# Performance work log

Measured on AMD Instinct MI355X. Metric: run time of the kernel, lower is better.

## Reference

```python
import jax, jax.numpy as jnp
import numpy as np

N_HEADS = 8
D_K = 64
SCALE = D_K ** (-0.5)


def setup_inputs() -> dict:
    key = jax.random.key(0)
    k1, k2, k3 = jax.random.split(key, 3)
    B, C, H, W = 8, 512, 32, 32
    x = jax.random.normal(k1, (B, C, H, W), dtype=jnp.float32)
    # Linear weights stored as [in, out] so y = x @ W + b (same math as torch Linear)
    W_qkv = jax.random.normal(k2, (C, N_HEADS * D_K * 3), dtype=jnp.float32) * (1.0 / np.sqrt(C))
    b_qkv = jnp.zeros((N_HEADS * D_K * 3,), dtype=jnp.float32)
    W_out = jax.random.normal(k3, (N_HEADS * D_K, C), dtype=jnp.float32) * (1.0 / np.sqrt(N_HEADS * D_K))
    b_out = jnp.zeros((C,), dtype=jnp.float32)
    return {"x": x, "W_qkv": W_qkv, "b_qkv": b_qkv, "W_out": W_out, "b_out": b_out}


def reference(x, W_qkv, b_qkv, W_out, b_out):
    B, C, H, W = x.shape
    N = H * W
    # [B, C, H, W] -> [B, N, C]  (tokens are spatial positions)
    xf = jnp.transpose(x.reshape(B, C, N), (0, 2, 1))
    # NOTE: the original forward never applies self.norm, so neither do we.
    qkv = xf @ W_qkv + b_qkv                       # [B, N, 3*h*d]
    qkv = qkv.reshape(B, N, N_HEADS, 3 * D_K)
    q, k, v = jnp.split(qkv, 3, axis=-1)           # each [B, N, h, d]
    attn = jnp.einsum('bihd,bjhd->bijh', q, k) * SCALE
    attn = jax.nn.softmax(attn, axis=2)            # softmax over key index j
    res = jnp.einsum('bijh,bjhd->bihd', attn, v)   # [B, N, h, d]
    res = res.reshape(B, N, N_HEADS * D_K)
    res = res @ W_out + b_out
    res = res + xf                                 # residual
    res = jnp.transpose(res, (0, 2, 1)).reshape(B, C, H, W)
    return res
```

## Files before the change

### kernel.cpp

```cpp
#include <hip/hip_runtime.h>
#include <hip/hip_bf16.h>
#include <cstdint>

typedef __bf16 bf16;
typedef __attribute__((ext_vector_type(8))) __bf16 bf16x8;
typedef __attribute__((ext_vector_type(4))) __bf16 bf16x4;
typedef __attribute__((ext_vector_type(4))) float f32x4;

#define CEXP 0.1803368801111244f

__global__ __launch_bounds__(256) void prep_all(const float* __restrict__ x,
                                                const float* __restrict__ Wqkv,
                                                const float* __restrict__ Wout,
                                                bf16* __restrict__ xT,
                                                bf16* __restrict__ WqkvT,
                                                bf16* __restrict__ WoutT) {
  __shared__ bf16 t[32][33];
  const int z = blockIdx.z;
  const float* src;
  bf16* dst;
  int C;
  if (z < 8) {
    if (blockIdx.x >= 32) return;
    src = x + (size_t)z * 512 * 1024;
    dst = xT + (size_t)z * 1024 * 512;
    C = 1024;
  } else if (z == 8) {
    src = Wqkv; dst = WqkvT; C = 1536;
  } else {
    if (blockIdx.x >= 16) return;
    src = Wout; dst = WoutT; C = 512;
  }
  const int c0 = blockIdx.x * 32, r0 = blockIdx.y * 32;
  const int tx = threadIdx.x, ty = threadIdx.y;
#pragma unroll
  for (int i = 0; i < 4; ++i)
    t[ty + i * 8][tx] = (bf16)src[(size_t)(r0 + ty + i * 8) * C + c0 + tx];
  __syncthreads();
#pragma unroll
  for (int i = 0; i < 4; ++i)
    dst[(size_t)(c0 + ty + i * 8) * 512 + r0 + tx] = t[tx][ty + i * 8];
}

__global__ __launch_bounds__(256) void gemm_qkv(const bf16* __restrict__ xT,
                                                const bf16* __restrict__ WqkvT,
                                                const float* __restrict__ bqkv,
                                                bf16* __restrict__ Qb,
                                                bf16* __restrict__ Kb,
                                                bf16* __restrict__ Vb) {
  __shared__ bf16 As[128 * 72];
  __shared__ bf16 Bs[128 * 72];
  const int b = blockIdx.z;
  const int m0 = blockIdx.y * 128;
  const int co0 = blockIdx.x * 128;
  const int tid = threadIdx.x;
  const int w = tid >> 6, l = tid & 63;
  const int wr = w >> 1, wc = w & 1;
  const int quad = l >> 4, l16 = l & 15;

  const bf16* A = xT + (size_t)b * 1024 * 512;

  f32x4 acc[4][4];
#pragma unroll
  for (int i = 0; i < 4; ++i)
#pragma unroll
    for (int j = 0; j < 4; ++j) acc[i][j] = (f32x4){0.f, 0.f, 0.f, 0.f};

  const int srow = w * 32 + (l >> 3);
  const int scol = (l & 7) * 8;

  for (int kk = 0; kk < 8; ++kk) {
    const int k0 = kk * 64;
    bf16x8 av[4], bv[4];
#pragma unroll
    for (int i = 0; i < 4; ++i) {
      av[i] = *(const bf16x8*)&A[(size_t)(m0 + srow + i * 8) * 512 + k0 + scol];
      bv[i] = *(const bf16x8*)&WqkvT[(size_t)(co0 + srow + i * 8) * 512 + k0 + scol];
    }
#pragma unroll
    for (int i = 0; i < 4; ++i) {
      *(bf16x8*)&As[(srow + i * 8) * 72 + scol] = av[i];
      *(bf16x8*)&Bs[(srow + i * 8) * 72 + scol] = bv[i];
    }
    __syncthreads();
#pragma unroll
    for (int ks = 0; ks < 2; ++ks) {
      bf16x8 a[4], bb[4];
#pragma unroll
      for (int rb = 0; rb < 4; ++rb)
        a[rb] = *(const bf16x8*)&As[(wr * 64 + rb * 16 + l16) * 72 + ks * 32 + quad * 8];
#pragma unroll
      for (int cb = 0; cb < 4; ++cb)
        bb[cb] = *(const bf16x8*)&Bs[(wc * 64 + cb * 16 + l16) * 72 + ks * 32 + quad * 8];
#pragma unroll
      for (int rb = 0; rb < 4; ++rb)
#pragma unroll
        for (int cb = 0; cb < 4; ++cb)
          acc[rb][cb] = __builtin_amdgcn_mfma_f32_16x16x32_bf16(a[rb], bb[cb], acc[rb][cb], 0, 0, 0);
    }
    __syncthreads();
  }

#pragma unroll
  for (int cb = 0; cb < 4; ++cb) {
    const int co = co0 + wc * 64 + cb * 16 + l16;
    const int h = co / 192;
    const int rem = co - h * 192;
    const int part = rem >> 6;
    const int dd = rem & 63;
    const float bias = bqkv[co];
    if (part == 2) {
      bf16* base = Vb + ((size_t)(b * 8 + h) * 64 + dd) * 1024;
#pragma unroll
      for (int rb = 0; rb < 4; ++rb) {
        const int n = m0 + wr * 64 + rb * 16 + quad * 4;
        f32x4 v = acc[rb][cb];
        bf16x4 ov;
#pragma unroll
        for (int r = 0; r < 4; ++r) ov[r] = (bf16)(v[r] + bias);
        *(bf16x4*)&base[n] = ov;
      }
    } else {
      const float sc = (part == 0) ? CEXP : 1.0f;
      bf16* dst = (part == 0) ? Qb : Kb;
      bf16* base = dst + ((size_t)(b * 8 + h) * 1024) * 64 + dd;
#pragma unroll
      for (int rb = 0; rb < 4; ++rb) {
        const int n = m0 + wr * 64 + rb * 16 + quad * 4;
        f32x4 v = acc[rb][cb];
#pragma unroll
        for (int r = 0; r < 4; ++r) base[(size_t)(n + r) * 64] = (bf16)((v[r] + bias) * sc);
      }
    }
  }
}

__global__ __launch_bounds__(256) void attn_k(const bf16* __restrict__ Qb,
                                              const bf16* __restrict__ Kb,
                                              const bf16* __restrict__ Vb,
                                              bf16* __restrict__ Ob) {
  __shared__ bf16 Ks[128 * 72];
  __shared__ bf16 Vs[64 * 136];
  const int bh = blockIdx.x;
  const int b = bh >> 3, h = bh & 7;
  const int q0 = blockIdx.y * 128;
  const int tid = threadIdx.x;
  const int w = tid >> 6, l = tid & 63;
  const int quad = l >> 4, l16 = l & 15;

  const bf16* Qg = Qb + (size_t)bh * 1024 * 64;
  const bf16* Kg = Kb + (size_t)bh * 1024 * 64;
  const bf16* Vg = Vb + (size_t)bh * 64 * 1024;

  bf16x8 qb[2][2];
#pragma unroll
  for (int mt = 0; mt < 2; ++mt)
#pragma unroll
    for (int ks = 0; ks < 2; ++ks)
      qb[mt][ks] = *(const bf16x8*)&Qg[(size_t)(q0 + w * 32 + mt * 16 + l16) * 64 + ks * 32 + quad * 8];

  bf16x8 ones;
#pragma unroll
  for (int e = 0; e < 8; ++e) ones[e] = (bf16)1.0f;

  f32x4 o[2][4], acc_l[2];
#pragma unroll
  for (int mt = 0; mt < 2; ++mt) {
    acc_l[mt] = (f32x4){0.f, 0.f, 0.f, 0.f};
#pragma unroll
    for (int db = 0; db < 4; ++db) o[mt][db] = (f32x4){0.f, 0.f, 0.f, 0.f};
  }

  const int kr = tid >> 1, kc = (tid & 1) * 32;
  const int vr = tid >> 2, vc = (tid & 3) * 32;

  bf16x8 ka[4], va[4];
#pragma unroll
  for (int e = 0; e < 4; ++e) {
    ka[e] = *(const bf16x8*)&Kg[(size_t)kr * 64 + kc + e * 8];
    va[e] = *(const bf16x8*)&Vg[(size_t)vr * 1024 + vc + e * 8];
  }

  for (int kv = 0; kv < 8; ++kv) {
    __syncthreads();
#pragma unroll
    for (int e = 0; e < 4; ++e) {
      *(bf16x8*)&Ks[kr * 72 + kc + e * 8] = ka[e];
      *(bf16x8*)&Vs[vr * 136 + vc + e * 8] = va[e];
    }
    __syncthreads();
    if (kv < 7) {
      const int j0 = (kv + 1) * 128;
#pragma unroll
      for (int e = 0; e < 4; ++e) {
        ka[e] = *(const bf16x8*)&Kg[(size_t)(j0 + kr) * 64 + kc + e * 8];
        va[e] = *(const bf16x8*)&Vg[(size_t)vr * 1024 + j0 + vc + e * 8];
      }
    }

    f32x4 s[2][8];
#pragma unroll
    for (int mt = 0; mt < 2; ++mt)
#pragma unroll
      for (int jb = 0; jb < 8; ++jb) s[mt][jb] = (f32x4){0.f, 0.f, 0.f, 0.f};
#pragma unroll
    for (int ks = 0; ks < 2; ++ks) {
      bf16x8 kaf[8];
#pragma unroll
      for (int jb = 0; jb < 8; ++jb)
        kaf[jb] = *(const bf16x8*)&Ks[(jb * 16 + l16) * 72 + ks * 32 + quad * 8];
#pragma unroll
      for (int jb = 0; jb < 8; ++jb)
#pragma unroll
        for (int mt = 0; mt < 2; ++mt)
          s[mt][jb] = __builtin_amdgcn_mfma_f32_16x16x32_bf16(kaf[jb], qb[mt][ks], s[mt][jb], 0, 0, 0);
    }

#pragma unroll
    for (int kj = 0; kj < 4; ++kj) {
      bf16x8 bv[4];
#pragma unroll
      for (int db = 0; db < 4; ++db) {
        const bf16x4 lo = *(const bf16x4*)&Vs[(db * 16 + l16) * 136 + kj * 32 + quad * 4];
        const bf16x4 hi = *(const bf16x4*)&Vs[(db * 16 + l16) * 136 + kj * 32 + 16 + quad * 4];
#pragma unroll
        for (int e = 0; e < 4; ++e) {
          bv[db][e] = lo[e];
          bv[db][4 + e] = hi[e];
        }
      }
#pragma unroll
      for (int mt = 0; mt < 2; ++mt) {
        bf16x8 ap;
#pragma unroll
        for (int rr = 0; rr < 4; ++rr) {
          ap[rr] = (bf16)__builtin_amdgcn_exp2f(s[mt][2 * kj][rr]);
          ap[4 + rr] = (bf16)__builtin_amdgcn_exp2f(s[mt][2 * kj + 1][rr]);
        }
        acc_l[mt] = __builtin_amdgcn_mfma_f32_16x16x32_bf16(ap, ones, acc_l[mt], 0, 0, 0);
#pragma unroll
        for (int db = 0; db < 4; ++db)
          o[mt][db] = __builtin_amdgcn_mfma_f32_16x16x32_bf16(ap, bv[db], o[mt][db], 0, 0, 0);
      }
    }
  }

  bf16* Og = Ob + (size_t)b * 1024 * 512 + h * 64;
#pragma unroll
  for (int mt = 0; mt < 2; ++mt) {
    f32x4 inv;
#pragma unroll
    for (int rr = 0; rr < 4; ++rr) inv[rr] = 1.0f / acc_l[mt][rr];
#pragma unroll
    for (int db = 0; db < 4; ++db)
#pragma unroll
      for (int rr = 0; rr < 4; ++rr) {
        const int n = q0 + w * 32 + mt * 16 + quad * 4 + rr;
        Og[(size_t)n * 512 + db * 16 + l16] = (bf16)(o[mt][db][rr] * inv[rr]);
      }
  }
}

__global__ __launch_bounds__(256) void gemm_out(const bf16* __restrict__ Ob,
                                                const bf16* __restrict__ WoutT,
                                                const float* __restrict__ bout,
                                                const float* __restrict__ x,
                                                float* __restrict__ out) {
  __shared__ bf16 As[128 * 72];
  __shared__ bf16 Bs[64 * 72];
  const int b = blockIdx.z;
  const int m0 = blockIdx.y * 128;
  const int co0 = blockIdx.x * 64;
  const int tid = threadIdx.x;
  const int w = tid >> 6, l = tid & 63;
  const int wr = w >> 1, wc = w & 1;
  const int quad = l >> 4, l16 = l & 15;

  const bf16* A = Ob + (size_t)b * 1024 * 512;

  f32x4 acc[4][2];
#pragma unroll
  for (int i = 0; i < 4; ++i)
#pragma unroll
    for (int j = 0; j < 2; ++j) acc[i][j] = (f32x4){0.f, 0.f, 0.f, 0.f};

  const int srow = w * 32 + (l >> 3);
  const int scol = (l & 7) * 8;
  const int brow = tid >> 2;
  const int bcol = (tid & 3) * 16;

  for (int kk = 0; kk < 8; ++kk) {
    const int k0 = kk * 64;
    bf16x8 av[4], bv[2];
#pragma unroll
    for (int i = 0; i < 4; ++i)
      av[i] = *(const bf16x8*)&A[(size_t)(m0 + srow + i * 8) * 512 + k0 + scol];
#pragma unroll
    for (int i = 0; i < 2; ++i)
      bv[i] = *(const bf16x8*)&WoutT[(size_t)(co0 + brow) * 512 + k0 + bcol + i * 8];
#pragma unroll
    for (int i = 0; i < 4; ++i)
      *(bf16x8*)&As[(srow + i * 8) * 72 + scol] = av[i];
#pragma unroll
    for (int i = 0; i < 2; ++i)
      *(bf16x8*)&Bs[brow * 72 + bcol + i * 8] = bv[i];
    __syncthreads();
#pragma unroll
    for (int ks = 0; ks < 2; ++ks) {
      bf16x8 a[4], bb[2];
#pragma unroll
      for (int rb = 0; rb < 4; ++rb)
        a[rb] = *(const bf16x8*)&As[(wr * 64 + rb * 16 + l16) * 72 + ks * 32 + quad * 8];
#pragma unroll
      for (int cb = 0; cb < 2; ++cb)
        bb[cb] = *(const bf16x8*)&Bs[(wc * 32 + cb * 16 + l16) * 72 + ks * 32 + quad * 8];
#pragma unroll
      for (int rb = 0; rb < 4; ++rb)
#pragma unroll
        for (int cb = 0; cb < 2; ++cb)
          acc[rb][cb] = __builtin_amdgcn_mfma_f32_16x16x32_bf16(a[rb], bb[cb], acc[rb][cb], 0, 0, 0);
    }
    __syncthreads();
  }

#pragma unroll
  for (int cb = 0; cb < 2; ++cb) {
    const int c = co0 + wc * 32 + cb * 16 + l16;
    const float bias = bout[c];
#pragma unroll
    for (int rb = 0; rb < 4; ++rb) {
      const int n = m0 + wr * 64 + rb * 16 + quad * 4;
      const size_t off = ((size_t)b * 512 + c) * 1024 + n;
      f32x4 res = *(const f32x4*)&x[off];
      f32x4 v = acc[rb][cb];
      f32x4 ov;
#pragma unroll
      for (int r = 0; r < 4; ++r) ov[r] = v[r] + bias + res[r];
      *(f32x4*)&out[off] = ov;
    }
  }
}

extern "C" void kernel_launch(void* const* d_in, const int* in_sizes, int n_in,
                              void* d_out, int out_size, void* d_ws, size_t ws_size,
                              hipStream_t stream) {
  const float* x = (const float*)d_in[0];
  const float* Wqkv = (const float*)d_in[1];
  const float* bqkv = (const float*)d_in[2];
  const float* Wout = (const float*)d_in[3];
  const float* bout = (const float*)d_in[4];
  float* out = (float*)d_out;
  char* ws = (char*)d_ws;

  const size_t MB = 1024 * 1024;
  bf16* xT = (bf16*)(ws);
  bf16* Ob = xT;
  bf16* Qbuf = (bf16*)(ws + 8 * MB);
  bf16* Kbuf = (bf16*)(ws + 16 * MB);
  bf16* Vbuf = (bf16*)(ws + 24 * MB);
  bf16* WqkvT = (bf16*)(ws + 32 * MB);
  bf16* WoutT = (bf16*)(ws + 32 * MB + 1572864);
  if (ws_size < 32 * MB + 1572864 + 524288) return;

  prep_all<<<dim3(48, 16, 10), dim3(32, 8), 0, stream>>>(x, Wqkv, Wout, xT, WqkvT, WoutT);
  gemm_qkv<<<dim3(12, 8, 8), 256, 0, stream>>>(xT, WqkvT, bqkv, Qbuf, Kbuf, Vbuf);
  attn_k<<<dim3(64, 8), 256, 0, stream>>>(Qbuf, Kbuf, Vbuf, Ob);
  gemm_out<<<dim3(8, 8, 8), 256, 0, stream>>>(Ob, WoutT, bout, x, out);
}
```

Measured before the change: 145.6 us.

## Pre-pack weights into MFMA fragment layout and load B operands directly from global

The prep kernel now writes the QKV and output-projection weights in a 16x32 fragment-packed layout, so each lane can load its MFMA B operand straight from global memory. Both GEMMs drop the shared-memory B tile and prefetch the next A tile into registers while the current one is consumed. Launch bounds now request 3 blocks per SM. This removes LDS traffic and one barrier stage for B, at the cost of more global loads per wave (B fragments are re-read by each row-warp) and higher register pressure.

```diff
diff --git a/kernel.cpp b/kernel.cpp
--- a/kernel.cpp
+++ b/kernel.cpp
@@ -9,47 +9,59 @@
 
 #define CEXP 0.1803368801111244f
 
+
 __global__ __launch_bounds__(256) void prep_all(const float* __restrict__ x,
                                                 const float* __restrict__ Wqkv,
                                                 const float* __restrict__ Wout,
                                                 bf16* __restrict__ xT,
-                                                bf16* __restrict__ WqkvT,
-                                                bf16* __restrict__ WoutT) {
+                                                bf16* __restrict__ WqkvP,
+                                                bf16* __restrict__ WoutP) {
   __shared__ bf16 t[32][33];
   const int z = blockIdx.z;
+  const int c0 = blockIdx.x * 32, r0 = blockIdx.y * 32;
+  const int tx = threadIdx.x, ty = threadIdx.y;
+
+  if (z < 8) {
+    const float* src = x + (size_t)z * 512 * 1024;
+    bf16* dst = xT + (size_t)z * 1024 * 512;
+    if (blockIdx.x >= 32) return;
+#pragma unroll
+    for (int i = 0; i < 4; ++i)
+      t[ty + i * 8][tx] = (bf16)src[(size_t)(r0 + ty + i * 8) * 1024 + c0 + tx];
+    __syncthreads();
+#pragma unroll
+    for (int i = 0; i < 4; ++i)
+      dst[(size_t)(c0 + ty + i * 8) * 512 + r0 + tx] = t[tx][ty + i * 8];
+    return;
+  }
   const float* src;
-  bf16* dst;
+  bf16* dstp;
   int C;
-  if (z < 8) {
-    if (blockIdx.x >= 32) return;
-    src = x + (size_t)z * 512 * 1024;
-    dst = xT + (size_t)z * 1024 * 512;
-    C = 1024;
-  } else if (z == 8) {
-    src = Wqkv; dst = WqkvT; C = 1536;
+  if (z == 8) {
+    src = Wqkv; dstp = WqkvP; C = 1536;
   } else {
     if (blockIdx.x >= 16) return;
-    src = Wout; dst = WoutT; C = 512;
-  }
-  const int c0 = blockIdx.x * 32, r0 = blockIdx.y * 32;
-  const int tx = threadIdx.x, ty = threadIdx.y;
+    src = Wout; dstp = WoutP; C = 512;
+  }
 #pragma unroll
   for (int i = 0; i < 4; ++i)
     t[ty + i * 8][tx] = (bf16)src[(size_t)(r0 + ty + i * 8) * C + c0 + tx];
   __syncthreads();
 #pragma unroll
-  for (int i = 0; i < 4; ++i)
-    dst[(size_t)(c0 + ty + i * 8) * 512 + r0 + tx] = t[tx][ty + i * 8];
-}
-
-__global__ __launch_bounds__(256) void gemm_qkv(const bf16* __restrict__ xT,
-                                                const bf16* __restrict__ WqkvT,
-                                                const float* __restrict__ bqkv,
-                                                bf16* __restrict__ Qb,
-                                                bf16* __restrict__ Kb,
-                                                bf16* __restrict__ Vb) {
+  for (int i = 0; i < 4; ++i) {
+    const int co = c0 + ty + i * 8;
+    dstp[(size_t)((co >> 4) * 16 + (r0 >> 5)) * 512 + (co & 15) * 32 + tx] =
+        t[tx][ty + i * 8];
+  }
+}
+
+__global__ __launch_bounds__(256, 3) void gemm_qkv(const bf16* __restrict__ xT,
+                                                   const bf16* __restrict__ WqkvP,
+                                                   const float* __restrict__ bqkv,
+                                                   bf16* __restrict__ Qb,
+                                                   bf16* __restrict__ Kb,
+                                                   bf16* __restrict__ Vb) {
   __shared__ bf16 As[128 * 72];
-  __shared__ bf16 Bs[128 * 72];
   const int b = blockIdx.z;
   const int m0 = blockIdx.y * 128;
   const int co0 = blockIdx.x * 128;
@@ -68,37 +80,44 @@
 
   const int srow = w * 32 + (l >> 3);
   const int scol = (l & 7) * 8;
+  const int lfrag = l16 * 32 + quad * 8;
+
+  bf16x8 av[4];
+#pragma unroll
+  for (int i = 0; i < 4; ++i)
+    av[i] = *(const bf16x8*)&A[(size_t)(m0 + srow + i * 8) * 512 + scol];
 
   for (int kk = 0; kk < 8; ++kk) {
-    const int k0 = kk * 64;
-    bf16x8 av[4], bv[4];
-#pragma unroll
-    for (int i = 0; i < 4; ++i) {
-      av[i] = *(const bf16x8*)&A[(size_t)(m0 + srow + i * 8) * 512 + k0 + scol];
-      bv[i] = *(const bf16x8*)&WqkvT[(size_t)(co0 + srow + i * 8) * 512 + k0 + scol];
-    }
-#pragma unroll
-    for (int i = 0; i < 4; ++i) {
+    __syncthreads();
+#pragma unroll
+    for (int i = 0; i < 4; ++i)
       *(bf16x8*)&As[(srow + i * 8) * 72 + scol] = av[i];
-      *(bf16x8*)&Bs[(srow + i * 8) * 72 + scol] = bv[i];
-    }
-    __syncthreads();
+    __syncthreads();
+    if (kk < 7) {
+      const int k0 = (kk + 1) * 64;
+#pragma unroll
+      for (int i = 0; i < 4; ++i)
+        av[i] = *(const bf16x8*)&A[(size_t)(m0 + srow + i * 8) * 512 + k0 + scol];
+    }
+    bf16x8 bb[2][4];
+#pragma unroll
+    for (int ks = 0; ks < 2; ++ks)
+#pragma unroll
+      for (int cb = 0; cb < 4; ++cb)
+        bb[ks][cb] = *(const bf16x8*)&WqkvP[(size_t)(((co0 >> 4) + wc * 4 + cb) * 16 +
+                                                     kk * 2 + ks) * 512 + lfrag];
 #pragma unroll
     for (int ks = 0; ks < 2; ++ks) {
-      bf16x8 a[4], bb[4];
+      bf16x8 a[4];
 #pragma unroll
       for (int rb = 0; rb < 4; ++rb)
         a[rb] = *(const bf16x8*)&As[(wr * 64 + rb * 16 + l16) * 72 + ks * 32 + quad * 8];
 #pragma unroll
-      for (int cb = 0; cb < 4; ++cb)
-        bb[cb] = *(const bf16x8*)&Bs[(wc * 64 + cb * 16 + l16) * 72 + ks * 32 + quad * 8];
-#pragma unroll
       for (int rb = 0; rb < 4; ++rb)
 #pragma unroll
         for (int cb = 0; cb < 4; ++cb)
-          acc[rb][cb] = __builtin_amdgcn_mfma_f32_16x16x32_bf16(a[rb], bb[cb], acc[rb][cb], 0, 0, 0);
-    }
-    __syncthreads();
+          acc[rb][cb] = __builtin_amdgcn_mfma_f32_16x16x32_bf16(a[rb], bb[ks][cb], acc[rb][cb], 0, 0, 0);
+    }
   }
 
 #pragma unroll
@@ -261,13 +280,12 @@
   }
 }
 
-__global__ __launch_bounds__(256) void gemm_out(const bf16* __restrict__ Ob,
-                                                const bf16* __restrict__ WoutT,
-                                                const float* __restrict__ bout,
-                                                const float* __restrict__ x,
-                                                float* __restrict__ out) {
+__global__ __launch_bounds__(256, 3) void gemm_out(const bf16* __restrict__ Ob,
+                                                   const bf16* __restrict__ WoutP,
+                                                   const float* __restrict__ bout,
+                                                   const float* __restrict__ x,
+                                                   float* __restrict__ out) {
   __shared__ bf16 As[128 * 72];
-  __shared__ bf16 Bs[64 * 72];
   const int b = blockIdx.z;
   const int m0 = blockIdx.y * 128;
   const int co0 = blockIdx.x * 64;
@@ -286,41 +304,44 @@
 
   const int srow = w * 32 + (l >> 3);
   const int scol = (l & 7) * 8;
-  const int brow = tid >> 2;
-  const int bcol = (tid & 3) * 16;
+  const int lfrag = l16 * 32 + quad * 8;
+
+  bf16x8 av[4];
+#pragma unroll
+  for (int i = 0; i < 4; ++i)
+    av[i] = *(const bf16x8*)&A[(size_t)(m0 + srow + i * 8) * 512 + scol];
 
   for (int kk = 0; kk < 8; ++kk) {
-    const int k0 = kk * 64;
-    bf16x8 av[4], bv[2];
-#pragma unroll
-    for (int i = 0; i < 4; ++i)
-      av[i] = *(const bf16x8*)&A[(size_t)(m0 + srow + i * 8) * 512 + k0 + scol];
-#pragma unroll
-    for (int i = 0; i < 2; ++i)
-      bv[i] = *(const bf16x8*)&WoutT[(size_t)(co0 + brow) * 512 + k0 + bcol + i * 8];
+    __syncthreads();
 #pragma unroll
     for (int i = 0; i < 4; ++i)
       *(bf16x8*)&As[(srow + i * 8) * 72 + scol] = av[i];
-#pragma unroll
-    for (int i = 0; i < 2; ++i)
-      *(bf16x8*)&Bs[brow * 72 + bcol + i * 8] = bv[i];
-    __syncthreads();
+    __syncthreads();
+    if (kk < 7) {
+      const int k0 = (kk + 1) * 64;
+#pragma unroll
+      for (int i = 0; i < 4; ++i)
+        av[i] = *(const bf16x8*)&A[(size_t)(m0 + srow + i * 8) * 512 + k0 + scol];
+    }
+    bf16x8 bb[2][2];
+#pragma unroll
+    for (int ks = 0; ks < 2; ++ks)
+#pragma unroll
+      for (int cb = 0; cb < 2; ++cb)
+        bb[ks][cb] = *(const bf16x8*)&WoutP[(size_t)(((co0 >> 4) + wc * 2 + cb) * 16 +
+                                                     kk * 2 + ks) * 512 + lfrag];
 #pragma unroll
     for (int ks = 0; ks < 2; ++ks) {
-      bf16x8 a[4], bb[2];
+      bf16x8 a[4];
 #pragma unroll
       for (int rb = 0; rb < 4; ++rb)
         a[rb] = *(const bf16x8*)&As[(wr * 64 + rb * 16 + l16) * 72 + ks * 32 + quad * 8];
 #pragma unroll
-      for (int cb = 0; cb < 2; ++cb)
-        bb[cb] = *(const bf16x8*)&Bs[(wc * 32 + cb * 16 + l16) * 72 + ks * 32 + quad * 8];
-#pragma unroll
       for (int rb = 0; rb < 4; ++rb)
 #pragma unroll
         for (int cb = 0; cb < 2; ++cb)
-          acc[rb][cb] = __builtin_amdgcn_mfma_f32_16x16x32_bf16(a[rb], bb[cb], acc[rb][cb], 0, 0, 0);
-    }
-    __syncthreads();
+          acc[rb][cb] = __builtin_amdgcn_mfma_f32_16x16x32_bf16(a[rb], bb[ks][cb], acc[rb][cb], 0, 0, 0);
+    }
   }
 
 #pragma unroll
@@ -358,12 +379,12 @@
   bf16* Qbuf = (bf16*)(ws + 8 * MB);
   bf16* Kbuf = (bf16*)(ws + 16 * MB);
   bf16* Vbuf = (bf16*)(ws + 24 * MB);
-  bf16* WqkvT = (bf16*)(ws + 32 * MB);
-  bf16* WoutT = (bf16*)(ws + 32 * MB + 1572864);
+  bf16* WqkvP = (bf16*)(ws + 32 * MB);
+  bf16* WoutP = (bf16*)(ws + 32 * MB + 1572864);
   if (ws_size < 32 * MB + 1572864 + 524288) return;
 
-  prep_all<<<dim3(48, 16, 10), dim3(32, 8), 0, stream>>>(x, Wqkv, Wout, xT, WqkvT, WoutT);
-  gemm_qkv<<<dim3(12, 8, 8), 256, 0, stream>>>(xT, WqkvT, bqkv, Qbuf, Kbuf, Vbuf);
+  prep_all<<<dim3(48, 16, 10), dim3(32, 8), 0, stream>>>(x, Wqkv, Wout, xT, WqkvP, WoutP);
+  gemm_qkv<<<dim3(12, 8, 8), 256, 0, stream>>>(xT, WqkvP, bqkv, Qbuf, Kbuf, Vbuf);
   attn_k<<<dim3(64, 8), 256, 0, stream>>>(Qbuf, Kbuf, Vbuf, Ob);
-  gemm_out<<<dim3(8, 8, 8), 256, 0, stream>>>(Ob, WoutT, bout, x, out);
-}
+  gemm_out<<<dim3(8, 8, 8), 256, 0, stream>>>(Ob, WoutP, bout, x, out);
+}
```

Measured after the change: 144.2 us. No clear change (-1.0%).
